# Performance work log

Hardware: AMD Instinct MI355X
Metric: run time of the kernel (lower is better)

The kernel has to match this reference:

```python
import jax, jax.numpy as jnp
import numpy as np

N_OBS = 8_000_000
N_PTS = 1_000_000
N_CAMS = 2_000


def setup_inputs() -> dict:
    key = jax.random.key(0)
    k1, k2, k3, k4, k5 = jax.random.split(key, 5)
    points_2d = jax.random.normal(k1, (N_OBS, 2), dtype=jnp.float32) * 100.0
    pose = jax.random.normal(k2, (N_CAMS, 7), dtype=jnp.float32)
    points_3d = jax.random.normal(k3, (N_PTS, 3), dtype=jnp.float32)
    camera_indices = jax.random.randint(k4, (N_OBS,), 0, N_CAMS, dtype=jnp.int64)
    point_indices = jax.random.randint(k5, (N_OBS,), 0, N_PTS, dtype=jnp.int64)
    # pinhole intrinsics: fx=fy=1000, cx=cy=500
    K = jnp.array([[1000.0, 0.0, 500.0],
                   [0.0, 1000.0, 500.0],
                   [0.0, 0.0, 1.0]], dtype=jnp.float32)
    return {"points_2d": points_2d, "K": K, "pose": pose,
            "points_3d": points_3d, "camera_indices": camera_indices,
            "point_indices": point_indices}


def rotate_quat(points, cam7):
    # cam7[:, :4] = quaternion (w, x, y, z), cam7[:, 4:7] = translation
    q = cam7[:, :4]
    q = q / jnp.linalg.norm(q, axis=-1, keepdims=True)
    w, qv = q[:, :1], q[:, 1:]            # [N,1], [N,3]
    uv = 2.0 * jnp.cross(qv, points)      # [N,3]
    rotated = points + w * uv + jnp.cross(qv, uv)
    return rotated + cam7[:, 4:7]


def homo2cart(p):
    return p[:, :2] / p[:, 2:3]


def reference(points_2d, K, pose, points_3d, camera_indices, point_indices):
    pts = points_3d[point_indices]        # gather [N_OBS,3]
    cam = pose[camera_indices]            # gather [N_OBS,7]
    points_proj = rotate_quat(pts, cam)
    pixels = points_proj @ K.T            # [N_OBS,3]
    pixels = homo2cart(pixels)            # [N_OBS,2]
    return pixels - points_2d
```

## Files before the change

### kernel.cpp

```cpp
#include <hip/hip_runtime.h>


typedef int   i32x2 __attribute__((ext_vector_type(2)));
typedef float f32x4 __attribute__((ext_vector_type(4)));
typedef float f32x4a __attribute__((ext_vector_type(4), aligned(4)));

__global__ void __launch_bounds__(256, 8)
reproj_kernel(const f32x4* __restrict__ p2d,
              const float* __restrict__ K,
              const float* __restrict__ pose,
              const float* __restrict__ pts3d,
              const i32x2* __restrict__ camIdx,
              const i32x2* __restrict__ ptIdx,
              f32x4*       __restrict__ out,
              int nPairs, int nPts)
{
    int i = blockIdx.x * blockDim.x + threadIdx.x;
    if (i >= nPairs) return;

    i32x2 ci = __builtin_nontemporal_load(&camIdx[i]);
    i32x2 pi = __builtin_nontemporal_load(&ptIdx[i]);
    f32x4 p  = __builtin_nontemporal_load(&p2d[i]);

    float K00 = K[0], K01 = K[1], K02 = K[2];
    float K10 = K[3], K11 = K[4], K12 = K[5];
    float K20 = K[6], K21 = K[7], K22 = K[8];

    auto project = [&](int c, int pidx, float& ox, float& oy) {
        f32x4 q4 = *(const f32x4a*)(pose + 7 * c);
        f32x4 t4 = *(const f32x4a*)(pose + 7 * c + 3);
        float qw = q4.x, qx = q4.y, qy = q4.z, qz = q4.w;
        float tx = t4.y, ty = t4.z, tz = t4.w;

        float inv = 1.0f / sqrtf(qw*qw + qx*qx + qy*qy + qz*qz);
        qw *= inv; qx *= inv; qy *= inv; qz *= inv;

        float x, y, z;
        if (pidx < nPts - 1) {
            f32x4 v = *(const f32x4a*)(pts3d + 3 * pidx);
            x = v.x; y = v.y; z = v.z;
        } else {
            f32x4 v = *(const f32x4a*)(pts3d + 3 * pidx - 1);
            x = v.y; y = v.z; z = v.w;
        }

        float uvx = 2.0f * (qy*z - qz*y);
        float uvy = 2.0f * (qz*x - qx*z);
        float uvz = 2.0f * (qx*y - qy*x);

        float rx = x + qw*uvx + (qy*uvz - qz*uvy) + tx;
        float ry = y + qw*uvy + (qz*uvx - qx*uvz) + ty;
        float rz = z + qw*uvz + (qx*uvy - qy*uvx) + tz;

        float px = K00*rx + K01*ry + K02*rz;
        float py = K10*rx + K11*ry + K12*rz;
        float pz = K20*rx + K21*ry + K22*rz;

        ox = px / pz;
        oy = py / pz;
    };

    float ax, ay, bx, by;
    project(ci.x, pi.x, ax, ay);
    project(ci.y, pi.y, bx, by);

    f32x4 r;
    r.x = ax - p.x; r.y = ay - p.y; r.z = bx - p.z; r.w = by - p.w;
    __builtin_nontemporal_store(r, &out[i]);
}

extern "C" void kernel_launch(void* const* d_in, const int* in_sizes, int n_in,
                              void* d_out, int out_size, void* d_ws, size_t ws_size,
                              hipStream_t stream)
{
    const float* points_2d = (const float*)d_in[0];
    const float* K         = (const float*)d_in[1];
    const float* pose      = (const float*)d_in[2];
    const float* points_3d = (const float*)d_in[3];
    const int*   camIdx    = (const int*)d_in[4];
    const int*   ptIdx     = (const int*)d_in[5];
    float*       out       = (float*)d_out;

    int nObs   = in_sizes[4];
    int nPairs = nObs / 2;
    int nPts   = in_sizes[3] / 3;

    const int block = 256;
    int grid = (nPairs + block - 1) / block;

    reproj_kernel<<<grid, block, 0, stream>>>(
        (const f32x4*)points_2d, K, pose, points_3d,
        (const i32x2*)camIdx, (const i32x2*)ptIdx,
        (f32x4*)out, nPairs, nPts);
}
```

Before: 268.0 us.

## Pre-pack poses and points into aligned 16-byte records and process four observations per thread

```diff
diff --git a/kernel.cpp b/kernel.cpp
--- a/kernel.cpp
+++ b/kernel.cpp
@@ -1,19 +1,102 @@
 #include <hip/hip_runtime.h>
 
 
-typedef int   i32x2 __attribute__((ext_vector_type(2)));
+typedef int   i32x4 __attribute__((ext_vector_type(4)));
 typedef float f32x4 __attribute__((ext_vector_type(4)));
 typedef float f32x4a __attribute__((ext_vector_type(4), aligned(4)));
+typedef int   i32x2 __attribute__((ext_vector_type(2)));
+
+__global__ void prep_pose(const float* __restrict__ pose,
+                          float* __restrict__ pose8, int nCams)
+{
+    int r = blockIdx.x * blockDim.x + threadIdx.x;
+    if (r >= nCams) return;
+    const float* src = pose + 7 * r;
+    float qw = src[0], qx = src[1], qy = src[2], qz = src[3];
+    float inv = 1.0f / sqrtf(qw*qw + qx*qx + qy*qy + qz*qz);
+    f32x4 q; q.x = qw*inv; q.y = qx*inv; q.z = qy*inv; q.w = qz*inv;
+    f32x4 t; t.x = src[4]; t.y = src[5]; t.z = src[6]; t.w = 0.0f;
+    *(f32x4*)(pose8 + 8*r)     = q;
+    *(f32x4*)(pose8 + 8*r + 4) = t;
+}
+
+__global__ void prep_pts(const float* __restrict__ pts3,
+                         float* __restrict__ pts4, int nPts)
+{
+    int r = blockIdx.x * blockDim.x + threadIdx.x;
+    if (r >= nPts) return;
+    f32x4 v;
+    v.x = pts3[3*r]; v.y = pts3[3*r + 1]; v.z = pts3[3*r + 2]; v.w = 0.0f;
+    *(f32x4*)(pts4 + 4*r) = v;
+}
 
 __global__ void __launch_bounds__(256, 8)
-reproj_kernel(const f32x4* __restrict__ p2d,
-              const float* __restrict__ K,
-              const float* __restrict__ pose,
-              const float* __restrict__ pts3d,
-              const i32x2* __restrict__ camIdx,
-              const i32x2* __restrict__ ptIdx,
-              f32x4*       __restrict__ out,
-              int nPairs, int nPts)
+reproj_main(const f32x4* __restrict__ p2d,
+            const float* __restrict__ K,
+            const f32x4* __restrict__ pose8,
+            const f32x4* __restrict__ pts4,
+            const i32x4* __restrict__ camIdx,
+            const i32x4* __restrict__ ptIdx,
+            f32x4*       __restrict__ out,
+            int nQuads)
+{
+    int i = blockIdx.x * blockDim.x + threadIdx.x;
+    if (i >= nQuads) return;
+
+    i32x4 ci = __builtin_nontemporal_load(&camIdx[i]);
+    i32x4 pi = __builtin_nontemporal_load(&ptIdx[i]);
+    f32x4 pA = __builtin_nontemporal_load(&p2d[2*i]);
+    f32x4 pB = __builtin_nontemporal_load(&p2d[2*i + 1]);
+
+    float K00 = K[0], K01 = K[1], K02 = K[2];
+    float K10 = K[3], K11 = K[4], K12 = K[5];
+    float K20 = K[6], K21 = K[7], K22 = K[8];
+
+    auto project = [&](int c, int pidx, float& ox, float& oy) {
+        f32x4 q4 = pose8[2*c];
+        f32x4 t4 = pose8[2*c + 1];
+        f32x4 v  = pts4[pidx];
+        float qw = q4.x, qx = q4.y, qy = q4.z, qz = q4.w;
+        float x = v.x, y = v.y, z = v.z;
+
+        float uvx = 2.0f * (qy*z - qz*y);
+        float uvy = 2.0f * (qz*x - qx*z);
+        float uvz = 2.0f * (qx*y - qy*x);
+
+        float rx = x + qw*uvx + (qy*uvz - qz*uvy) + t4.x;
+        float ry = y + qw*uvy + (qz*uvx - qx*uvz) + t4.y;
+        float rz = z + qw*uvz + (qx*uvy - qy*uvx) + t4.z;
+
+        float px = K00*rx + K01*ry + K02*rz;
+        float py = K10*rx + K11*ry + K12*rz;
+        float pz = K20*rx + K21*ry + K22*rz;
+
+        ox = px / pz;
+        oy = py / pz;
+    };
+
+    float x0,y0,x1,y1,x2,y2,x3,y3;
+    project(ci.x, pi.x, x0, y0);
+    project(ci.y, pi.y, x1, y1);
+    project(ci.z, pi.z, x2, y2);
+    project(ci.w, pi.w, x3, y3);
+
+    f32x4 rA, rB;
+    rA.x = x0 - pA.x; rA.y = y0 - pA.y; rA.z = x1 - pA.z; rA.w = y1 - pA.w;
+    rB.x = x2 - pB.x; rB.y = y2 - pB.y; rB.z = x3 - pB.z; rB.w = y3 - pB.w;
+    __builtin_nontemporal_store(rA, &out[2*i]);
+    __builtin_nontemporal_store(rB, &out[2*i + 1]);
+}
+
+__global__ void __launch_bounds__(256, 8)
+reproj_fallback(const f32x4* __restrict__ p2d,
+                const float* __restrict__ K,
+                const float* __restrict__ pose,
+                const float* __restrict__ pts3d,
+                const i32x2* __restrict__ camIdx,
+                const i32x2* __restrict__ ptIdx,
+                f32x4*       __restrict__ out,
+                int nPairs, int nPts)
 {
     int i = blockIdx.x * blockDim.x + threadIdx.x;
     if (i >= nPairs) return;
@@ -27,8 +110,8 @@
     float K20 = K[6], K21 = K[7], K22 = K[8];
 
     auto project = [&](int c, int pidx, float& ox, float& oy) {
-        f32x4 q4 = *(const f32x4a*)(pose + 7 * c);
-        f32x4 t4 = *(const f32x4a*)(pose + 7 * c + 3);
+        f32x4 q4 = *(const f32x4a*)(pose + 7*c);
+        f32x4 t4 = *(const f32x4a*)(pose + 7*c + 3);
         float qw = q4.x, qx = q4.y, qy = q4.z, qz = q4.w;
         float tx = t4.y, ty = t4.z, tz = t4.w;
 
@@ -37,10 +120,10 @@
 
         float x, y, z;
         if (pidx < nPts - 1) {
-            f32x4 v = *(const f32x4a*)(pts3d + 3 * pidx);
+            f32x4 v = *(const f32x4a*)(pts3d + 3*pidx);
             x = v.x; y = v.y; z = v.z;
         } else {
-            f32x4 v = *(const f32x4a*)(pts3d + 3 * pidx - 1);
+            f32x4 v = *(const f32x4a*)(pts3d + 3*pidx - 1);
             x = v.y; y = v.z; z = v.w;
         }
 
@@ -78,18 +161,38 @@
     const float* pose      = (const float*)d_in[2];
     const float* points_3d = (const float*)d_in[3];
     const int*   camIdx    = (const int*)d_in[4];
-    const int*   ptIdx     = (const int*)d_in[5];
+    const int*   ptIdx    = (const int*)d_in[5];
     float*       out       = (float*)d_out;
 
-    int nObs   = in_sizes[4];
-    int nPairs = nObs / 2;
-    int nPts   = in_sizes[3] / 3;
+    int nObs  = in_sizes[4];
+    int nCams = in_sizes[2] / 7;
+    int nPts  = in_sizes[3] / 3;
+
+    size_t poseBytes = (size_t)nCams * 8 * sizeof(float);
+    size_t ptsOff    = 65536;
+    size_t needed    = ptsOff + (size_t)nPts * 4 * sizeof(float);
 
     const int block = 256;
-    int grid = (nPairs + block - 1) / block;
 
-    reproj_kernel<<<grid, block, 0, stream>>>(
-        (const f32x4*)points_2d, K, pose, points_3d,
-        (const i32x2*)camIdx, (const i32x2*)ptIdx,
-        (f32x4*)out, nPairs, nPts);
+    if (ws_size >= needed && nObs % 4 == 0 && poseBytes <= ptsOff) {
+        float* pose8 = (float*)d_ws;
+        float* pts4  = (float*)((char*)d_ws + ptsOff);
+
+        prep_pose<<<(nCams + block - 1) / block, block, 0, stream>>>(pose, pose8, nCams);
+        prep_pts<<<(nPts + block - 1) / block, block, 0, stream>>>(points_3d, pts4, nPts);
+
+        int nQuads = nObs / 4;
+        int grid = (nQuads + block - 1) / block;
+        reproj_main<<<grid, block, 0, stream>>>(
+            (const f32x4*)points_2d, K, (const f32x4*)pose8, (const f32x4*)pts4,
+            (const i32x4*)camIdx, (const i32x4*)ptIdx,
+            (f32x4*)out, nQuads);
+    } else {
+        int nPairs = nObs / 2;
+        int grid = (nPairs + block - 1) / block;
+        reproj_fallback<<<grid, block, 0, stream>>>(
+            (const f32x4*)points_2d, K, pose, points_3d,
+            (const i32x2*)camIdx, (const i32x2*)ptIdx,
+            (f32x4*)out, nPairs, nPts);
+    }
 }
```

Result: slower. 295.0 us (+10.1%).
